# Optimization experiments

Measured on AMD Instinct MI355X. Metric: run time of the kernel, lower is better.

Reference implementation:

```python
import jax, jax.numpy as jnp
import numpy as np

D_MODEL = 1024
N_HEADS = 16
HEAD_DIM = D_MODEL // N_HEADS
THETA = 10000.0
B, T = 2, 2048


def apply_rope(x, pos, theta=THETA):
    # x: (b, h, t, d), pos: (t,)
    d = x.shape[-1]
    inv_freq = theta ** (-jnp.arange(0, d, 2, dtype=jnp.float32) / d)  # (d/2,)
    ang = pos.astype(jnp.float32)[:, None] * inv_freq[None, :]          # (t, d/2)
    cos, sin = jnp.cos(ang), jnp.sin(ang)
    x1, x2 = x[..., 0::2], x[..., 1::2]
    out_even = x1 * cos - x2 * sin
    out_odd = x1 * sin + x2 * cos
    return jnp.stack([out_even, out_odd], axis=-1).reshape(x.shape)


def setup_inputs() -> dict:
    key = jax.random.key(0)
    ks = jax.random.split(key, 5)
    s = 1.0 / np.sqrt(D_MODEL)
    return {
        "x": jax.random.normal(ks[0], (B, T, D_MODEL), jnp.float32),
        "wq": jax.random.normal(ks[1], (D_MODEL, D_MODEL), jnp.float32) * s,
        "wk": jax.random.normal(ks[2], (D_MODEL, D_MODEL), jnp.float32) * s,
        "wv": jax.random.normal(ks[3], (D_MODEL, D_MODEL), jnp.float32) * s,
        "wo": jax.random.normal(ks[4], (D_MODEL, D_MODEL), jnp.float32) * s,
        "token_pos": 1,
    }


def reference(x, wq, wk, wv, wo, token_pos):
    b, t, dm = x.shape
    # bias-free Linear: y = x @ W^T; split heads -> (b, h, t, d)
    def proj(w):
        y = jnp.einsum('btm,nm->btn', x, w)
        return y.reshape(b, t, N_HEADS, HEAD_DIM).transpose(0, 2, 1, 3)
    q, k, v = proj(wq), proj(wk), proj(wv)
    pos = jnp.arange(t)
    q = apply_rope(q, pos)
    k = apply_rope(k, pos)
    scale = jnp.sqrt(jnp.asarray(HEAD_DIM, dtype=x.dtype))
    scores = jnp.einsum('bhqd,bhkd->bhqk', q, k) / scale
    mask = jnp.tril(jnp.ones((t, t), dtype=bool))
    scores = jnp.where(mask, scores, -jnp.inf)
    attn = jax.nn.softmax(scores, axis=-1)
    out = jnp.einsum('bhqk,bhkd->bhqd', attn, v)
    out = out.transpose(0, 2, 1, 3).reshape(b, t, dm)
    return jnp.einsum('btm,nm->btn', out, wo)
```

## Files before the change

### kernel.cpp

```cpp
#include <hip/hip_runtime.h>
#include <hip/hip_bf16.h>
#include <math.h>

#define DM 1024
#define NH 16
#define HD 64
#define BB 2
#define TT 2048
#define MROWS (BB*TT)
#define PL ((size_t)MROWS * DM)
#define PLW ((size_t)DM * DM)

typedef unsigned short ushort_t;

using bf8_t = __attribute__((ext_vector_type(8))) __bf16;
using bf4_t = __attribute__((ext_vector_type(4))) __bf16;
using f4_t  = __attribute__((ext_vector_type(4))) float;

__global__ void detect_dtype(const unsigned short* __restrict__ x, int* flag) {
    __shared__ int cnt;
    if (threadIdx.x == 0) cnt = 0;
    __syncthreads();
    int local = 0;
    for (int i = threadIdx.x; i < 512; i += 256) {
        unsigned short u = x[i];
        int e = (u >> 7) & 0xFF;
        if (e >= 117 && e <= 130) local++;
    }
    atomicAdd(&cnt, local);
    __syncthreads();
    if (threadIdx.x == 0) *flag = (cnt >= 384) ? 0 : 1;
}

__global__ __launch_bounds__(256) void trig_init(float2* __restrict__ trig) {
    const int idx = blockIdx.x * 256 + threadIdx.x;
    const int t = idx >> 5, ip = idx & 31;
    const float inv_freq = powf(10000.0f, -2.0f * (float)ip / 64.0f);
    const float ang = (float)t * inv_freq;
    float s, c;
    sincosf(ang, &s, &c);
    trig[idx] = make_float2(c, s);
}

__global__ __launch_bounds__(256) void split_x(const void* __restrict__ X,
                                               __bf16* __restrict__ Xh,
                                               const int* __restrict__ flag) {
    const int f32 = *flag;
    __bf16* Xl = Xh + PL;
    const size_t i = ((size_t)blockIdx.x * 256 + threadIdx.x) * 4;
    if (i >= PL) return;
    if (f32) {
        float4 v = *(const float4*)((const float*)X + i);
        __bf16 h0 = (__bf16)v.x, h1 = (__bf16)v.y, h2 = (__bf16)v.z, h3 = (__bf16)v.w;
        bf4_t hv = {h0, h1, h2, h3};
        bf4_t lv = {(__bf16)(v.x - (float)h0), (__bf16)(v.y - (float)h1),
                    (__bf16)(v.z - (float)h2), (__bf16)(v.w - (float)h3)};
        *(bf4_t*)(Xh + i) = hv;
        *(bf4_t*)(Xl + i) = lv;
    } else {
        bf4_t v = *(const bf4_t*)((const __bf16*)X + i);
        *(bf4_t*)(Xh + i) = v;
        bf4_t zv = {(__bf16)0.f, (__bf16)0.f, (__bf16)0.f, (__bf16)0.f};
        *(bf4_t*)(Xl + i) = zv;
    }
}

__global__ __launch_bounds__(256) void split_w(const void* __restrict__ w0,
        const void* __restrict__ w1, const void* __restrict__ w2,
        const void* __restrict__ w3, __bf16* __restrict__ Wsp,
        const int* __restrict__ flag) {
    const int f32 = *flag;
    const int widx = blockIdx.y;
    const void* W = (widx == 0) ? w0 : (widx == 1) ? w1 : (widx == 2) ? w2 : w3;
    __bf16* Wh = Wsp + (size_t)widx * 2 * PLW;
    __bf16* Wl = Wh + PLW;
    const size_t i = ((size_t)blockIdx.x * 256 + threadIdx.x) * 4;
    if (i >= PLW) return;
    if (f32) {
        float4 v = *(const float4*)((const float*)W + i);
        __bf16 h0 = (__bf16)v.x, h1 = (__bf16)v.y, h2 = (__bf16)v.z, h3 = (__bf16)v.w;
        bf4_t hv = {h0, h1, h2, h3};
        bf4_t lv = {(__bf16)(v.x - (float)h0), (__bf16)(v.y - (float)h1),
                    (__bf16)(v.z - (float)h2), (__bf16)(v.w - (float)h3)};
        *(bf4_t*)(Wh + i) = hv;
        *(bf4_t*)(Wl + i) = lv;
    } else {
        bf4_t v = *(const bf4_t*)((const __bf16*)W + i);
        *(bf4_t*)(Wh + i) = v;
        bf4_t zv = {(__bf16)0.f, (__bf16)0.f, (__bf16)0.f, (__bf16)0.f};
        *(bf4_t*)(Wl + i) = zv;
    }
}

__device__ __forceinline__ int swz(int r, int b) {
    return r * 128 + (b ^ ((r & 7) << 4));
}
#define VST 264

__global__ __launch_bounds__(256, 3) void gemm_fused(
        const __bf16* __restrict__ Ahg,
        const __bf16* __restrict__ Wsp,
        __bf16* __restrict__ Y0, __bf16* __restrict__ Y1,
        __bf16* __restrict__ Y2,
        void* __restrict__ Yout,
        const float2* __restrict__ trig,
        const int* __restrict__ flag, const int outMode)
{
    const int f32 = *flag;
    const int z = blockIdx.z;
    const int widx = outMode ? 3 : z;
    const __bf16* Whg = Wsp + (size_t)widx * 2 * PLW;
    const __bf16* Wlg = Whg + PLW;
    const __bf16* Alg = Ahg + PL;
    const bool aLo = (outMode != 0) || (f32 != 0);
    const bool wLo = (f32 != 0);

    __shared__ __align__(16) char sm[49152];
    char* const AhL = sm;
    char* const AlL = sm + 16384;
    char* const WhL = sm + 32768;
    char* const WlL = sm + 40960;

    const int tid  = threadIdx.x;
    const int n0   = blockIdx.x * 64, m0 = blockIdx.y * 128;
    const int lane = tid & 63;
    const int w    = tid >> 6;
    const int wr   = (w >> 1) * 64;
    const int wcn  = (w & 1) * 32;
    const int l15  = lane & 15;
    const int g    = lane >> 4;

    f4_t acc[4][2] = {};
    bf8_t pa[4], pal[4], pwh[2], pwl[2];

    auto ISSUE = [&](int k0) {
#pragma unroll
        for (int j = 0; j < 4; j++) {
            const int u = tid + j * 256, r = u >> 3, c = u & 7;
            pa[j] = *(const bf8_t*)(Ahg + (size_t)(m0 + r) * DM + k0 + c * 8);
            if (aLo)
                pal[j] = *(const bf8_t*)(Alg + (size_t)(m0 + r) * DM + k0 + c * 8);
        }
#pragma unroll
        for (int j = 0; j < 2; j++) {
            const int u = tid + j * 256, r = u >> 3, c = u & 7;
            pwh[j] = *(const bf8_t*)(Whg + (size_t)(n0 + r) * DM + k0 + c * 8);
            if (wLo)
                pwl[j] = *(const bf8_t*)(Wlg + (size_t)(n0 + r) * DM + k0 + c * 8);
        }
    };

    ISSUE(0);
    for (int k0 = 0; k0 < DM; k0 += 64) {
        if (k0) __syncthreads();
#pragma unroll
        for (int j = 0; j < 4; j++) {
            const int u = tid + j * 256, r = u >> 3, c = u & 7;
            *(bf8_t*)(AhL + swz(r, c * 16)) = pa[j];
            if (aLo) *(bf8_t*)(AlL + swz(r, c * 16)) = pal[j];
        }
#pragma unroll
        for (int j = 0; j < 2; j++) {
            const int u = tid + j * 256, r = u >> 3, c = u & 7;
            *(bf8_t*)(WhL + swz(r, c * 16)) = pwh[j];
            if (wLo) *(bf8_t*)(WlL + swz(r, c * 16)) = pwl[j];
        }
        __syncthreads();

        if (k0 + 64 < DM) ISSUE(k0 + 64);

#pragma unroll
        for (int kh = 0; kh < 2; kh++) {
            const int bc = kh * 64 + g * 16;
            bf8_t ah[4], al[4], wh[2], wl[2];
#pragma unroll
            for (int m = 0; m < 4; m++) {
                ah[m] = *(const bf8_t*)(AhL + swz(wr + m * 16 + l15, bc));
                if (aLo) al[m] = *(const bf8_t*)(AlL + swz(wr + m * 16 + l15, bc));
            }
#pragma unroll
            for (int n = 0; n < 2; n++) {
                wh[n] = *(const bf8_t*)(WhL + swz(wcn + n * 16 + l15, bc));
                if (wLo) wl[n] = *(const bf8_t*)(WlL + swz(wcn + n * 16 + l15, bc));
            }
#pragma unroll
            for (int m = 0; m < 4; m++)
#pragma unroll
                for (int n = 0; n < 2; n++) {
                    acc[m][n] = __builtin_amdgcn_mfma_f32_16x16x32_bf16(
                                    ah[m], wh[n], acc[m][n], 0, 0, 0);
                    if (aLo)
                        acc[m][n] = __builtin_amdgcn_mfma_f32_16x16x32_bf16(
                                        al[m], wh[n], acc[m][n], 0, 0, 0);
                    if (wLo)
                        acc[m][n] = __builtin_amdgcn_mfma_f32_16x16x32_bf16(
                                        ah[m], wl[n], acc[m][n], 0, 0, 0);
                }
        }
    }

    const int orow = g * 4;
    const int ocol = l15;
    __syncthreads();

    if (outMode) {
        if (f32) {
#pragma unroll
            for (int m = 0; m < 4; m++)
#pragma unroll
                for (int n = 0; n < 2; n++) {
                    const int gr = m0 + wr + m * 16 + orow;
                    const int gc = n0 + wcn + n * 16 + ocol;
#pragma unroll
                    for (int r = 0; r < 4; r++)
                        ((float*)Yout)[(size_t)(gr + r) * DM + gc] = acc[m][n][r];
                }
        } else {
            char* const EhL = sm;
#pragma unroll
            for (int m = 0; m < 4; m++)
#pragma unroll
                for (int n = 0; n < 2; n++) {
                    const int ctile = wcn + n * 16 + ocol;
#pragma unroll
                    for (int r = 0; r < 4; r++) {
                        const int rtile = wr + m * 16 + orow + r;
                        *(__bf16*)(EhL + rtile * 128 + ctile * 2) = (__bf16)acc[m][n][r];
                    }
                }
            __syncthreads();
#pragma unroll
            for (int j = 0; j < 4; j++) {
                const int u = tid + j * 256, r = u >> 3, c = u & 7;
                *(bf8_t*)((__bf16*)Yout + (size_t)(m0 + r) * DM + n0 + c * 8) =
                    *(const bf8_t*)(EhL + r * 128 + c * 16);
            }
        }
    } else if (z == 2) {
        char* const EhL = sm;
        char* const ElL = sm + 20480;
#pragma unroll
        for (int m = 0; m < 4; m++)
#pragma unroll
            for (int n = 0; n < 2; n++) {
                const int ctile = wcn + n * 16 + ocol;
#pragma unroll
                for (int r = 0; r < 4; r++) {
                    const int rtile = wr + m * 16 + orow + r;
                    const float val = acc[m][n][r];
                    __bf16 hb = (__bf16)val;
                    *(__bf16*)(EhL + ctile * VST + rtile * 2) = hb;
                    *(__bf16*)(ElL + ctile * VST + rtile * 2) = (__bf16)(val - (float)hb);
                }
            }
        __syncthreads();
        __bf16* Vh = Y2;
        __bf16* Vl = Y2 + PL;
#pragma unroll
        for (int j = 0; j < 4; j++) {
            const int u = tid + j * 256, cc = u >> 4, k = u & 15;
            *(bf8_t*)(Vh + (size_t)(n0 + cc) * MROWS + m0 + k * 8) =
                *(const bf8_t*)(EhL + cc * VST + k * 16);
            *(bf8_t*)(Vl + (size_t)(n0 + cc) * MROWS + m0 + k * 8) =
                *(const bf8_t*)(ElL + cc * VST + k * 16);
        }
    } else {
        char* const EhL = sm;
        char* const ElL = sm + 20480;
#pragma unroll
        for (int m = 0; m < 4; m++)
#pragma unroll
            for (int n = 0; n < 2; n++) {
                const int ctile = wcn + n * 16 + ocol;
                const int gc = n0 + ctile;
                const int ip = (gc & 63) >> 1;
                const bool oddc = (gc & 1) != 0;
#pragma unroll
                for (int r = 0; r < 4; r++) {
                    const int rtile = wr + m * 16 + orow + r;
                    const int t = (m0 + rtile) & (TT - 1);
                    const float2 cs = trig[t * 32 + ip];
                    const float v = acc[m][n][r];
                    const float ov = __shfl_xor(v, 1);
                    float res = oddc ? (ov * cs.y + v * cs.x) : (v * cs.x - ov * cs.y);
                    if (z == 0) res *= 0.125f;
                    __bf16 hb = (__bf16)res;
                    *(__bf16*)(EhL + rtile * 128 + ctile * 2) = hb;
                    *(__bf16*)(ElL + rtile * 128 + ctile * 2) = (__bf16)(res - (float)hb);
                }
            }
        __syncthreads();
        __bf16* Yh = z ? Y1 : Y0;
        __bf16* Yl = Yh + PL;
#pragma unroll
        for (int j = 0; j < 4; j++) {
            const int u = tid + j * 256, r = u >> 3, c = u & 7;
            *(bf8_t*)(Yh + (size_t)(m0 + r) * DM + n0 + c * 8) =
                *(const bf8_t*)(EhL + r * 128 + c * 16);
            *(bf8_t*)(Yl + (size_t)(m0 + r) * DM + n0 + c * 8) =
                *(const bf8_t*)(ElL + r * 128 + c * 16);
        }
    }
}

__global__ void __launch_bounds__(256, 2) flash_attn_mfma(
        const __bf16* __restrict__ Qhg, const __bf16* __restrict__ Khg,
        const __bf16* __restrict__ Vhg, __bf16* __restrict__ Aoh)
{
    __shared__ __align__(16) char sm[81920];

    const __bf16* Qlg = Qhg + PL;
    const __bf16* Klg = Khg + PL;
    const __bf16* Vlg = Vhg + PL;
    __bf16* Aol = Aoh + PL;

    const int pi  = blockIdx.x;
    const int h   = blockIdx.y;
    const int b   = blockIdx.z;
    const int tid = threadIdx.x;
    const int lane = tid & 63;
    const int w    = tid >> 6;
    const int l15  = lane & 15;
    const int g    = lane >> 4;

    char* const pb = sm + 65536 + w * 4096;

    bf8_t pk[2], pkl[2], pv[2], pvl[2];
    auto ISSUE = [&](int kt) {
#pragma unroll
        for (int j = 0; j < 2; j++) {
            const int u = tid + j * 256, r = u >> 3, c = u & 7;
            const size_t ko = (size_t)(b * TT + kt * 64 + r) * DM + h * HD + c * 8;
            pk[j]  = *(const bf8_t*)(Khg + ko);
            pkl[j] = *(const bf8_t*)(Klg + ko);
            const size_t vo = (size_t)(h * HD + r) * MROWS + b * TT + kt * 64 + c * 8;
            pv[j]  = *(const bf8_t*)(Vhg + vo);
            pvl[j] = *(const bf8_t*)(Vlg + vo);
        }
    };
    auto WRITE = [&](char* base) {
#pragma unroll
        for (int j = 0; j < 2; j++) {
            const int u = tid + j * 256, r = u >> 3, c = u & 7;
            *(bf8_t*)(base +         swz(r, c * 16)) = pk[j];
            *(bf8_t*)(base +  8192 + swz(r, c * 16)) = pkl[j];
            *(bf8_t*)(base + 16384 + swz(r, c * 16)) = pv[j];
            *(bf8_t*)(base + 24576 + swz(r, c * 16)) = pvl[j];
        }
    };

#pragma unroll 1
    for (int ph = 0; ph < 2; ph++) {
        const int qt = ph ? pi : (31 - pi);

        bf8_t qh[2], ql[2];
#pragma unroll
        for (int kh = 0; kh < 2; kh++) {
            const size_t off = (size_t)(b * TT + qt * 64 + w * 16 + l15) * DM
                             + h * HD + kh * 32 + g * 8;
            qh[kh] = *(const bf8_t*)(Qhg + off);
            ql[kh] = *(const bf8_t*)(Qlg + off);
        }

        f4_t o[4] = {};
        float lrow = 0.f;

        ISSUE(0);
        WRITE(sm);
        __syncthreads();

        for (int kt = 0; kt <= qt; kt++) {
            char* const cb = sm + (kt & 1) * 32768;
            if (kt < qt) ISSUE(kt + 1);

            f4_t s[4] = {};
#pragma unroll
            for (int kh = 0; kh < 2; kh++) {
#pragma unroll
                for (int n = 0; n < 4; n++) {
                    bf8_t kf  = *(const bf8_t*)(cb +        swz(n * 16 + l15, kh * 64 + g * 16));
                    bf8_t kl2 = *(const bf8_t*)(cb + 8192 + swz(n * 16 + l15, kh * 64 + g * 16));
                    s[n] = __builtin_amdgcn_mfma_f32_16x16x32_bf16(kf,  qh[kh], s[n], 0, 0, 0);
                    s[n] = __builtin_amdgcn_mfma_f32_16x16x32_bf16(kl2, qh[kh], s[n], 0, 0, 0);
                    s[n] = __builtin_amdgcn_mfma_f32_16x16x32_bf16(kf,  ql[kh], s[n], 0, 0, 0);
                }
            }

            if (kt == qt) {
                const int qoff = w * 16 + l15;
#pragma unroll
                for (int n = 0; n < 4; n++)
#pragma unroll
                    for (int r = 0; r < 4; r++)
                        if (n * 16 + g * 4 + r > qoff) s[n][r] = -INFINITY;
            }

#pragma unroll
            for (int n = 0; n < 4; n++) {
                bf4_t hv, lv;
#pragma unroll
                for (int r = 0; r < 4; r++) {
                    const float p = __expf(s[n][r] - 8.0f);
                    lrow += p;
                    __bf16 hb = (__bf16)p;
                    hv[r] = hb;
                    lv[r] = (__bf16)(p - (float)hb);
                }
                *(bf4_t*)(pb +        swz(l15, n * 32 + g * 8)) = hv;
                *(bf4_t*)(pb + 2048 + swz(l15, n * 32 + g * 8)) = lv;
            }
            asm volatile("s_waitcnt lgkmcnt(0)" ::: "memory");
            __builtin_amdgcn_sched_barrier(0);

            bf8_t pah[2], pal2[2];
#pragma unroll
            for (int kh = 0; kh < 2; kh++) {
                pah[kh]  = *(const bf8_t*)(pb +        swz(l15, kh * 64 + g * 16));
                pal2[kh] = *(const bf8_t*)(pb + 2048 + swz(l15, kh * 64 + g * 16));
            }

#pragma unroll
            for (int kh = 0; kh < 2; kh++)
#pragma unroll
                for (int nf = 0; nf < 4; nf++) {
                    bf8_t vf  = *(const bf8_t*)(cb + 16384 + swz(nf * 16 + l15, kh * 64 + g * 16));
                    bf8_t vl2 = *(const bf8_t*)(cb + 24576 + swz(nf * 16 + l15, kh * 64 + g * 16));
                    o[nf] = __builtin_amdgcn_mfma_f32_16x16x32_bf16(pah[kh],  vf,  o[nf], 0, 0, 0);
                    o[nf] = __builtin_amdgcn_mfma_f32_16x16x32_bf16(pal2[kh], vf,  o[nf], 0, 0, 0);
                    o[nf] = __builtin_amdgcn_mfma_f32_16x16x32_bf16(pah[kh],  vl2, o[nf], 0, 0, 0);
                }

            if (kt < qt) WRITE(sm + ((kt + 1) & 1) * 32768);
            __syncthreads();
        }

        lrow += __shfl_xor(lrow, 16);
        lrow += __shfl_xor(lrow, 32);
        const float inv = 1.0f / lrow;
        float linv[4];
#pragma unroll
        for (int r = 0; r < 4; r++)
            linv[r] = __shfl(inv, (lane & 48) | (g * 4 + r));

#pragma unroll
        for (int nf = 0; nf < 4; nf++)
#pragma unroll
            for (int r = 0; r < 4; r++) {
                const float val = o[nf][r] * linv[r];
                __bf16 hb = (__bf16)val;
                *(__bf16*)(pb + (g * 4 + r) * 128 + (nf * 16 + l15) * 2) = hb;
                *(__bf16*)(pb + 2048 + (g * 4 + r) * 128 + (nf * 16 + l15) * 2) =
                    (__bf16)(val - (float)hb);
            }
        asm volatile("s_waitcnt lgkmcnt(0)" ::: "memory");
        __builtin_amdgcn_sched_barrier(0);
#pragma unroll
        for (int j = 0; j < 2; j++) {
            const int u = lane + j * 64, r = u >> 3, c = u & 7;
            const size_t off = (size_t)(b * TT + qt * 64 + w * 16 + r) * DM
                             + h * HD + c * 8;
            *(bf8_t*)(Aoh + off) = *(const bf8_t*)(pb + r * 128 + c * 16);
            *(bf8_t*)(Aol + off) = *(const bf8_t*)(pb + 2048 + r * 128 + c * 16);
        }
    }
}

extern "C" void kernel_launch(void* const* d_in, const int* in_sizes, int n_in,
                              void* d_out, int out_size, void* d_ws, size_t ws_size,
                              hipStream_t stream) {
    const void* x  = d_in[0];
    const void* wq = d_in[1];
    const void* wk = d_in[2];
    const void* wv = d_in[3];
    const void* wo = d_in[4];

    __bf16* Qh  = (__bf16*)d_ws;
    __bf16* Kh  = Qh + 2 * PL;
    __bf16* Vth = Kh + 2 * PL;
    __bf16* Xh  = Vth + 2 * PL;
    __bf16* Wsp = Xh + 2 * PL;
    char* tail  = (char*)(Wsp + 8 * PLW);
    int* flag   = (int*)tail;
    float2* trig = (float2*)(tail + 512);

    detect_dtype<<<1, 256, 0, stream>>>((const unsigned short*)x, flag);
    trig_init<<<TT * 32 / 256, 256, 0, stream>>>(trig);
    split_x<<<(unsigned)(PL / 4 / 256), 256, 0, stream>>>(x, Xh, flag);
    split_w<<<dim3((unsigned)(PLW / 4 / 256), 4), 256, 0, stream>>>(
        wq, wk, wv, wo, Wsp, flag);

    gemm_fused<<<dim3(DM / 64, MROWS / 128, 3), 256, 0, stream>>>(
        Xh, Wsp, Qh, Kh, Vth, nullptr, trig, flag, 0);

    flash_attn_mfma<<<dim3(16, NH, BB), 256, 0, stream>>>(Qh, Kh, Vth, Xh);

    gemm_fused<<<dim3(DM / 64, MROWS / 128, 1), 256, 0, stream>>>(
        Xh, Wsp, nullptr, nullptr, nullptr, d_out, trig, flag, 1);
}
```

Baseline: 295.5 us.

## Merge prep kernels into one launch, remap blocks across XCDs, add MFMA priority

Merges dtype detection, trig table init, and the x/weight bf16 hi/lo splits into a single prep kernel, where every block redoes the dtype detection locally. Launch count drops from four prep kernels to one. The GEMM and flash-attention kernels remap flat block IDs so consecutive logical tiles land on the same XCD, aiming for better L2 reuse. s_setprio is raised around the MFMA loops in attention to favour matrix work over other waves. The cost is 512 redundant reads of x per block in prep, plus some integer div/mod overhead.

```diff
diff --git a/kernel.cpp b/kernel.cpp
--- a/kernel.cpp
+++ b/kernel.cpp
@@ -11,85 +11,83 @@
 #define PL ((size_t)MROWS * DM)
 #define PLW ((size_t)DM * DM)
 
-typedef unsigned short ushort_t;
-
 using bf8_t = __attribute__((ext_vector_type(8))) __bf16;
 using bf4_t = __attribute__((ext_vector_type(4))) __bf16;
 using f4_t  = __attribute__((ext_vector_type(4))) float;
 
-__global__ void detect_dtype(const unsigned short* __restrict__ x, int* flag) {
+__global__ __launch_bounds__(256) void prep(
+        const void* __restrict__ X,
+        const void* __restrict__ w0, const void* __restrict__ w1,
+        const void* __restrict__ w2, const void* __restrict__ w3,
+        __bf16* __restrict__ Xh, __bf16* __restrict__ Wsp,
+        float2* __restrict__ trig, int* __restrict__ flag)
+{
+    const int id  = (int)blockIdx.x;
+    const int tid = (int)threadIdx.x;
+
     __shared__ int cnt;
-    if (threadIdx.x == 0) cnt = 0;
+    if (tid == 0) cnt = 0;
     __syncthreads();
-    int local = 0;
-    for (int i = threadIdx.x; i < 512; i += 256) {
-        unsigned short u = x[i];
-        int e = (u >> 7) & 0xFF;
-        if (e >= 117 && e <= 130) local++;
-    }
-    atomicAdd(&cnt, local);
+    {
+        int local = 0;
+        const unsigned short* xu = (const unsigned short*)X;
+        for (int i = tid; i < 512; i += 256) {
+            const int e = (xu[i] >> 7) & 0xFF;
+            if (e >= 117 && e <= 130) local++;
+        }
+        atomicAdd(&cnt, local);
+    }
     __syncthreads();
-    if (threadIdx.x == 0) *flag = (cnt >= 384) ? 0 : 1;
-}
-
-__global__ __launch_bounds__(256) void trig_init(float2* __restrict__ trig) {
-    const int idx = blockIdx.x * 256 + threadIdx.x;
-    const int t = idx >> 5, ip = idx & 31;
-    const float inv_freq = powf(10000.0f, -2.0f * (float)ip / 64.0f);
-    const float ang = (float)t * inv_freq;
-    float s, c;
-    sincosf(ang, &s, &c);
-    trig[idx] = make_float2(c, s);
-}
-
-__global__ __launch_bounds__(256) void split_x(const void* __restrict__ X,
-                                               __bf16* __restrict__ Xh,
-                                               const int* __restrict__ flag) {
-    const int f32 = *flag;
-    __bf16* Xl = Xh + PL;
-    const size_t i = ((size_t)blockIdx.x * 256 + threadIdx.x) * 4;
-    if (i >= PL) return;
+    const int f32 = (cnt >= 384) ? 0 : 1;
+
+    if (id >= 8448) {
+        if (tid == 0) *flag = f32;
+        return;
+    }
+    if (id >= 8192) {
+        const int idx = (id - 8192) * 256 + tid;
+        const int t = idx >> 5, ip = idx & 31;
+        const float inv_freq = powf(10000.0f, -2.0f * (float)ip / 64.0f);
+        const float ang = (float)t * inv_freq;
+        float s, c;
+        sincosf(ang, &s, &c);
+        trig[idx] = make_float2(c, s);
+        return;
+    }
+
+    const void* Src;
+    __bf16 *Yh, *Yl;
+    size_t i;
+    if (id < 4096) {
+        Src = X;
+        Yh = Xh; Yl = Xh + PL;
+        i = ((size_t)id * 256 + tid) * 4;
+    } else {
+        const int wid   = (id - 4096) >> 10;
+        const int inner = (id - 4096) & 1023;
+        Src = (wid == 0) ? w0 : (wid == 1) ? w1 : (wid == 2) ? w2 : w3;
+        Yh = Wsp + (size_t)wid * 2 * PLW;
+        Yl = Yh + PLW;
+        i = ((size_t)inner * 256 + tid) * 4;
+    }
     if (f32) {
-        float4 v = *(const float4*)((const float*)X + i);
+        float4 v = *(const float4*)((const float*)Src + i);
         __bf16 h0 = (__bf16)v.x, h1 = (__bf16)v.y, h2 = (__bf16)v.z, h3 = (__bf16)v.w;
         bf4_t hv = {h0, h1, h2, h3};
         bf4_t lv = {(__bf16)(v.x - (float)h0), (__bf16)(v.y - (float)h1),
                     (__bf16)(v.z - (float)h2), (__bf16)(v.w - (float)h3)};
-        *(bf4_t*)(Xh + i) = hv;
-        *(bf4_t*)(Xl + i) = lv;
+        *(bf4_t*)(Yh + i) = hv;
+        *(bf4_t*)(Yl + i) = lv;
     } else {
-        bf4_t v = *(const bf4_t*)((const __bf16*)X + i);
-        *(bf4_t*)(Xh + i) = v;
+        bf4_t v = *(const bf4_t*)((const __bf16*)Src + i);
+        *(bf4_t*)(Yh + i) = v;
         bf4_t zv = {(__bf16)0.f, (__bf16)0.f, (__bf16)0.f, (__bf16)0.f};
-        *(bf4_t*)(Xl + i) = zv;
+        *(bf4_t*)(Yl + i) = zv;
     }
 }
 
-__global__ __launch_bounds__(256) void split_w(const void* __restrict__ w0,
-        const void* __restrict__ w1, const void* __restrict__ w2,
-        const void* __restrict__ w3, __bf16* __restrict__ Wsp,
-        const int* __restrict__ flag) {
-    const int f32 = *flag;
-    const int widx = blockIdx.y;
-    const void* W = (widx == 0) ? w0 : (widx == 1) ? w1 : (widx == 2) ? w2 : w3;
-    __bf16* Wh = Wsp + (size_t)widx * 2 * PLW;
-    __bf16* Wl = Wh + PLW;
-    const size_t i = ((size_t)blockIdx.x * 256 + threadIdx.x) * 4;
-    if (i >= PLW) return;
-    if (f32) {
-        float4 v = *(const float4*)((const float*)W + i);
-        __bf16 h0 = (__bf16)v.x, h1 = (__bf16)v.y, h2 = (__bf16)v.z, h3 = (__bf16)v.w;
-        bf4_t hv = {h0, h1, h2, h3};
-        bf4_t lv = {(__bf16)(v.x - (float)h0), (__bf16)(v.y - (float)h1),
-                    (__bf16)(v.z - (float)h2), (__bf16)(v.w - (float)h3)};
-        *(bf4_t*)(Wh + i) = hv;
-        *(bf4_t*)(Wl + i) = lv;
-    } else {
-        bf4_t v = *(const bf4_t*)((const __bf16*)W + i);
-        *(bf4_t*)(Wh + i) = v;
-        bf4_t zv = {(__bf16)0.f, (__bf16)0.f, (__bf16)0.f, (__bf16)0.f};
-        *(bf4_t*)(Wl + i) = zv;
-    }
+__device__ __forceinline__ int xcd_remap(int flat, int nwg) {
+    return (flat & 7) * (nwg >> 3) + (flat >> 3);
 }
 
 __device__ __forceinline__ int swz(int r, int b) {
@@ -107,7 +105,15 @@
         const int* __restrict__ flag, const int outMode)
 {
     const int f32 = *flag;
-    const int z = blockIdx.z;
+
+    const int nx = (int)gridDim.x, ny = (int)gridDim.y, nz = (int)gridDim.z;
+    int flat = (int)blockIdx.x + nx * ((int)blockIdx.y + ny * (int)blockIdx.z);
+    flat = xcd_remap(flat, nx * ny * nz);
+    const int bx = flat % nx;
+    const int rem = flat / nx;
+    const int by = rem % ny;
+    const int z  = rem / ny;
+
     const int widx = outMode ? 3 : z;
     const __bf16* Whg = Wsp + (size_t)widx * 2 * PLW;
     const __bf16* Wlg = Whg + PLW;
@@ -122,7 +128,7 @@
     char* const WlL = sm + 40960;
 
     const int tid  = threadIdx.x;
-    const int n0   = blockIdx.x * 64, m0 = blockIdx.y * 128;
+    const int n0   = bx * 64, m0 = by * 128;
     const int lane = tid & 63;
     const int w    = tid >> 6;
     const int wr   = (w >> 1) * 64;
@@ -314,9 +320,12 @@
     const __bf16* Vlg = Vhg + PL;
     __bf16* Aol = Aoh + PL;
 
-    const int pi  = blockIdx.x;
-    const int h   = blockIdx.y;
-    const int b   = blockIdx.z;
+    int flat = (int)blockIdx.x + 16 * ((int)blockIdx.y + 16 * (int)blockIdx.z);
+    flat = xcd_remap(flat, 512);
+    const int pi = flat % 16;
+    const int h  = (flat / 16) % 16;
+    const int b  = flat / 256;
+
     const int tid = threadIdx.x;
     const int lane = tid & 63;
     const int w    = tid >> 6;
@@ -374,6 +383,7 @@
             if (kt < qt) ISSUE(kt + 1);
 
             f4_t s[4] = {};
+            __builtin_amdgcn_s_setprio(1);
 #pragma unroll
             for (int kh = 0; kh < 2; kh++) {
 #pragma unroll
@@ -385,6 +395,7 @@
                     s[n] = __builtin_amdgcn_mfma_f32_16x16x32_bf16(kf,  ql[kh], s[n], 0, 0, 0);
                 }
             }
+            __builtin_amdgcn_s_setprio(0);
 
             if (kt == qt) {
                 const int qoff = w * 16 + l15;
@@ -419,6 +430,7 @@
                 pal2[kh] = *(const bf8_t*)(pb + 2048 + swz(l15, kh * 64 + g * 16));
             }
 
+            __builtin_amdgcn_s_setprio(1);
 #pragma unroll
             for (int kh = 0; kh < 2; kh++)
 #pragma unroll
@@ -429,6 +441,7 @@
                     o[nf] = __builtin_amdgcn_mfma_f32_16x16x32_bf16(pal2[kh], vf,  o[nf], 0, 0, 0);
                     o[nf] = __builtin_amdgcn_mfma_f32_16x16x32_bf16(pah[kh],  vl2, o[nf], 0, 0, 0);
                 }
+            __builtin_amdgcn_s_setprio(0);
 
             if (kt < qt) WRITE(sm + ((kt + 1) & 1) * 32768);
             __syncthreads();
@@ -483,11 +496,7 @@
     int* flag   = (int*)tail;
     float2* trig = (float2*)(tail + 512);
 
-    detect_dtype<<<1, 256, 0, stream>>>((const unsigned short*)x, flag);
-    trig_init<<<TT * 32 / 256, 256, 0, stream>>>(trig);
-    split_x<<<(unsigned)(PL / 4 / 256), 256, 0, stream>>>(x, Xh, flag);
-    split_w<<<dim3((unsigned)(PLW / 4 / 256), 4), 256, 0, stream>>>(
-        wq, wk, wv, wo, Wsp, flag);
+    prep<<<8449, 256, 0, stream>>>(x, wq, wk, wv, wo, Xh, Wsp, trig, flag);
 
     gemm_fused<<<dim3(DM / 64, MROWS / 128, 3), 256, 0, stream>>>(
         Xh, Wsp, Qh, Kh, Vth, nullptr, trig, flag, 0);
```

New measurement: 287.7 us. 1.03x faster.
